# Kernel tuning notes

Hardware: AMD Instinct MI355X
Metric: run time of the kernel (lower is better)

Reference implementation:

```python
import jax, jax.numpy as jnp
import numpy as np
from jax.scipy.optimize import minimize

LAMDA = 0.01        # lamda default in MI()
N_DOMAINS = 2       # domain_label is binary (source/target)
MAXITER = 50        # BFGS iteration budget (torchmin l-bfgs analogue)


def _sq_dists(A, B):
    # squared euclidean pairwise distances == torch.cdist(A, B, p=2) ** 2
    an = jnp.sum(A * A, axis=-1)
    bn = jnp.sum(B * B, axis=-1)
    return an[:, None] + bn[None, :] - 2.0 * (A @ B.T)


def _median_sigma(sf):
    # sigma = median of nonzero squared pairwise source distances.
    # With continuous features the only zeros are the diagonal, so mask it.
    pd = jnp.maximum(_sq_dists(sf, sf), 0.0)
    pd = jnp.where(jnp.eye(pd.shape[0], dtype=bool), jnp.nan, pd)
    return jnp.nanmedian(pd)


def _build(sf, tf, y, l):
    # Gaussian kernel masked by class agreement, plus domain one-hots.
    sigma = _median_sigma(sf)
    X = jnp.concatenate([sf, tf], axis=0)              # [N, d]
    D = _sq_dists(X, X)                                 # [N, N]
    Deltay = (y[:, None] == y[None, :]).astype(X.dtype)
    K_W = jnp.exp(-D / sigma) * Deltay                  # [N, N]
    onehot = jax.nn.one_hot(l[:, 0], N_DOMAINS, dtype=X.dtype)  # [N, 2]
    KD = K_W * (onehot @ onehot.T)                      # K_W * Deltal
    w = jnp.sum(onehot, axis=0) / X.shape[0]            # domain counts / N
    return K_W, KD, onehot, w


def _div(theta, K_W, KD, onehot, w):
    # mean((K_W*Deltal) @ theta) - mean(exp((theta*K_W) @ Deltal - 1))
    # Deltal = onehot @ onehot.T (rank-2), so the second NxN @ NxN matmul
    # collapses to A = K_W @ (theta[:,None]*onehot) with column weights w.
    term1 = jnp.mean(KD @ theta)
    A = K_W @ (theta[:, None] * onehot)                 # [N, 2]
    term2 = jnp.mean(jnp.exp(A - 1.0) @ w)
    return term1 - term2


def _solve_theta(K_W, KD, onehot, w):
    N = K_W.shape[0]
    obj = lambda th: -_div(th, K_W, KD, onehot, w) + LAMDA * (th @ th)
    res = minimize(obj, jnp.zeros((N,), K_W.dtype), method="BFGS",
                   options={"maxiter": MAXITER})
    return res.x


def setup_inputs() -> dict:
    key = jax.random.key(0)
    k1, k2, k3, k4 = jax.random.split(key, 4)
    B, d, n_class = 2048, 256, 31
    source_features = jax.random.normal(k1, (B, d), dtype=jnp.float32)
    target_features = jax.random.normal(k2, (B, d), dtype=jnp.float32)
    y = jax.random.randint(k3, (2 * B,), 0, n_class, dtype=jnp.int32)
    l = jax.random.randint(k4, (2 * B, 1), 0, N_DOMAINS, dtype=jnp.int32)
    return {"source_features": source_features, "target_features": target_features,
            "y": y, "l": l}


def reference(source_features, target_features, y, l):
    K_W, KD, onehot, w = _build(source_features, target_features, y, l)
    theta_hat = _solve_theta(K_W, KD, onehot, w)
    return _div(theta_hat, K_W, KD, onehot, w)
```

## Files before the change

### kernel.cpp

```cpp
#include <hip/hip_runtime.h>
#include <math.h>

#define N_TOT   4096
#define N_SRC   2048
#define DIMF    256
#define NCLASS  31
#define LAMBDA  0.01f

#define K_TRI1  1048063LL
#define K_TRI2  1048064LL

#define WS_ACC    0
#define WS_HIST0  64
#define WS_HISTA  16448
#define WS_HISTB  32832
#define WS_H2A    49216
#define WS_H2B    50240
#define WS_STATE  51264
#define WS_TICK   51520
#define WS_META   52288
#define WS_SCAL   52800
#define ZERO_BYTES 53248
#define WS_PERM   53248
#define WS_XN     69632
#define WS_DS     1048576
#define WS_KBLK   17825792

#define MAXW 224
#define MAXM 112
#define WPAD 116

__device__ __forceinline__ float bf2f(unsigned short h) {
  return __uint_as_float(((unsigned)h) << 16);
}

__device__ __forceinline__ float wredF(float v) {
#pragma unroll
  for (int o = 1; o < 64; o <<= 1) v += __shfl_xor(v, o, 64);
  return v;
}

__device__ __forceinline__ double blockReduceSum(double v, double* red) {
#pragma unroll
  for (int o = 32; o > 0; o >>= 1) v += __shfl_down(v, o, 64);
  int w = threadIdx.x >> 6, lane = threadIdx.x & 63;
  __syncthreads();
  if (lane == 0) red[w] = v;
  __syncthreads();
  return red[0] + red[1] + red[2] + red[3];
}

__device__ __forceinline__ void blockReduceSumMax(double s, double mx, double* red,
                                                  double& os, double& om) {
#pragma unroll
  for (int o = 32; o > 0; o >>= 1) {
    s += __shfl_down(s, o, 64);
    double u = __shfl_down(mx, o, 64);
    mx = fmax(mx, u);
  }
  int w = threadIdx.x >> 6, lane = threadIdx.x & 63;
  __syncthreads();
  if (lane == 0) { red[w] = s; red[4 + w] = mx; }
  __syncthreads();
  os = red[0] + red[1] + red[2] + red[3];
  om = fmax(fmax(red[4], red[5]), fmax(red[6], red[7]));
}

__device__ void scan_find(const unsigned* hist, int nbins, long long k, unsigned* shOut) {
  __shared__ long long tsum[256];
  int tid = threadIdx.x;
  int per = nbins / 256;
  long long s = 0;
  for (int q = 0; q < per; q++) s += hist[tid * per + q];
  tsum[tid] = s;
  __syncthreads();
  long long acc = s;
  for (int off = 1; off < 256; off <<= 1) {
    long long add = (tid >= off) ? tsum[tid - off] : 0;
    __syncthreads();
    acc += add;
    tsum[tid] = acc;
    __syncthreads();
  }
  long long run = acc - s;
  for (int q = 0; q < per; q++) {
    unsigned c = hist[tid * per + q];
    if (k >= run && k < run + (long long)c) { shOut[0] = (unsigned)(tid * per + q); shOut[1] = (unsigned)(k - run); }
    run += c;
  }
  __syncthreads();
}

__global__ __launch_bounds__(256) void xn_kernel(const float* __restrict__ sf,
                                                 const float* __restrict__ tf,
                                                 float* __restrict__ xn) {
  int wid = threadIdx.x >> 6, lane = threadIdx.x & 63;
  int row = blockIdx.x * 4 + wid;
  const float* src = (row < N_SRC) ? (sf + (size_t)row * DIMF) : (tf + (size_t)(row - N_SRC) * DIMF);
  float4 v = ((const float4*)src)[lane];
  float s = v.x * v.x + v.y * v.y + v.z * v.z + v.w * v.w;
#pragma unroll
  for (int o = 32; o > 0; o >>= 1) s += __shfl_down(s, o, 64);
  if (lane == 0) xn[row] = s;
}

__global__ __launch_bounds__(256) void dist_k(const float* __restrict__ sf,
                                              const float* __restrict__ xn,
                                              float* __restrict__ Ds,
                                              unsigned* __restrict__ h) {
  __shared__ float As[16][68];
  __shared__ float Bs[16][68];
  __shared__ unsigned lh[4096];
  const int tx = threadIdx.x, ty = threadIdx.y;
  const int tid = ty * 16 + tx;
  for (int q = tid; q < 4096; q += 256) lh[q] = 0;
  int b = blockIdx.x;
  int by = (int)((sqrtf(8.f * (float)b + 1.f) - 1.f) * 0.5f);
  while ((by + 1) * (by + 2) / 2 <= b) ++by;
  while (by * (by + 1) / 2 > b) --by;
  int bx = b - by * (by + 1) / 2;
  const int R = by * 64, C = bx * 64;
  const int si = tid >> 2, sq = tid & 3;
  float4 va = ((const float4*)(sf + (size_t)(R + si) * 256 + 0))[sq];
  float4 vb = ((const float4*)(sf + (size_t)(C + si) * 256 + 0))[sq];
  float acc[4][4] = {};
  for (int kc = 0; kc < 256; kc += 16) {
    As[sq * 4 + 0][si] = va.x; As[sq * 4 + 1][si] = va.y; As[sq * 4 + 2][si] = va.z; As[sq * 4 + 3][si] = va.w;
    Bs[sq * 4 + 0][si] = vb.x; Bs[sq * 4 + 1][si] = vb.y; Bs[sq * 4 + 2][si] = vb.z; Bs[sq * 4 + 3][si] = vb.w;
    __syncthreads();
    if (kc + 16 < 256) {
      va = ((const float4*)(sf + (size_t)(R + si) * 256 + kc + 16))[sq];
      vb = ((const float4*)(sf + (size_t)(C + si) * 256 + kc + 16))[sq];
    }
#pragma unroll
    for (int k = 0; k < 16; k++) {
      float4 a = *(const float4*)&As[k][ty * 4];
      float4 b2 = *(const float4*)&Bs[k][tx * 4];
      acc[0][0] += a.x * b2.x; acc[0][1] += a.x * b2.y; acc[0][2] += a.x * b2.z; acc[0][3] += a.x * b2.w;
      acc[1][0] += a.y * b2.x; acc[1][1] += a.y * b2.y; acc[1][2] += a.y * b2.z; acc[1][3] += a.y * b2.w;
      acc[2][0] += a.z * b2.x; acc[2][1] += a.z * b2.y; acc[2][2] += a.z * b2.z; acc[2][3] += a.z * b2.w;
      acc[3][0] += a.w * b2.x; acc[3][1] += a.w * b2.y; acc[3][2] += a.w * b2.z; acc[3][3] += a.w * b2.w;
    }
    __syncthreads();
  }
  int jbase = C + tx * 4;
  float xnj0 = xn[jbase + 0], xnj1 = xn[jbase + 1], xnj2 = xn[jbase + 2], xnj3 = xn[jbase + 3];
#pragma unroll
  for (int r = 0; r < 4; r++) {
    int i = R + ty * 4 + r;
    float xni = xn[i];
    float v[4];
    v[0] = fmaxf(xni + xnj0 - 2.f * acc[r][0], 0.f);
    v[1] = fmaxf(xni + xnj1 - 2.f * acc[r][1], 0.f);
    v[2] = fmaxf(xni + xnj2 - 2.f * acc[r][2], 0.f);
    v[3] = fmaxf(xni + xnj3 - 2.f * acc[r][3], 0.f);
    if (jbase + 3 < i) {
      float4 o; o.x = v[0]; o.y = v[1]; o.z = v[2]; o.w = v[3];
      ((float4*)&Ds[(size_t)i * 2048 + jbase])[0] = o;
      atomicAdd(&lh[__float_as_uint(v[0]) >> 20], 1u);
      atomicAdd(&lh[__float_as_uint(v[1]) >> 20], 1u);
      atomicAdd(&lh[__float_as_uint(v[2]) >> 20], 1u);
      atomicAdd(&lh[__float_as_uint(v[3]) >> 20], 1u);
    } else {
#pragma unroll
      for (int k = 0; k < 4; k++) {
        if (jbase + k < i) {
          Ds[(size_t)i * 2048 + jbase + k] = v[k];
          atomicAdd(&lh[__float_as_uint(v[k]) >> 20], 1u);
        }
      }
    }
  }
  __syncthreads();
  for (int q = tid; q < 4096; q += 256) if (lh[q]) atomicAdd(&h[q], lh[q]);
}

__global__ __launch_bounds__(256) void scan0_k(const unsigned* __restrict__ h, unsigned* __restrict__ st) {
  __shared__ unsigned r0[2];
  __shared__ unsigned r1[2];
  scan_find(h, 4096, K_TRI1, r0);
  scan_find(h, 4096, K_TRI2, r1);
  if (threadIdx.x == 0) { st[0] = r0[0]; st[1] = r0[1]; st[2] = r1[0]; st[3] = r1[1]; }
}

__global__ __launch_bounds__(256) void hist1_k(const float* __restrict__ Ds, const unsigned* __restrict__ st,
                                               unsigned* __restrict__ hA, unsigned* __restrict__ hB) {
  __shared__ unsigned lA[4096];
  __shared__ unsigned lB[4096];
  for (int i = threadIdx.x; i < 4096; i += 256) { lA[i] = 0; lB[i] = 0; }
  __syncthreads();
  unsigned s0 = st[0], s1 = st[2];
  int gw = (blockIdx.x * 256 + threadIdx.x) >> 6;
  int lane = threadIdx.x & 63;
  const float* row = Ds + (size_t)gw * 2048;
  for (int j = lane; j < gw; j += 64) {
    unsigned u = __float_as_uint(row[j]);
    unsigned hi = u >> 20, mid = (u >> 8) & 0xFFFu;
    if (hi == s0) atomicAdd(&lA[mid], 1u);
    if (hi == s1) atomicAdd(&lB[mid], 1u);
  }
  __syncthreads();
  for (int i = threadIdx.x; i < 4096; i += 256) {
    if (lA[i]) atomicAdd(&hA[i], lA[i]);
    if (lB[i]) atomicAdd(&hB[i], lB[i]);
  }
}

__global__ __launch_bounds__(256) void scan1_k(const unsigned* __restrict__ hA, const unsigned* __restrict__ hB,
                                               unsigned* __restrict__ st) {
  __shared__ unsigned r0[2];
  __shared__ unsigned r1[2];
  long long kA = (long long)st[1];
  long long kB = (long long)st[3];
  scan_find(hA, 4096, kA, r0);
  scan_find(hB, 4096, kB, r1);
  if (threadIdx.x == 0) { st[4] = r0[0]; st[5] = r0[1]; st[6] = r1[0]; st[7] = r1[1]; }
}

__global__ __launch_bounds__(256) void hist2_k(const float* __restrict__ Ds, const unsigned* __restrict__ st,
                                               unsigned* __restrict__ hA, unsigned* __restrict__ hB) {
  __shared__ unsigned lA[256];
  __shared__ unsigned lB[256];
  lA[threadIdx.x] = 0; lB[threadIdx.x] = 0;
  __syncthreads();
  unsigned p0 = (st[0] << 12) | st[4];
  unsigned p1 = (st[2] << 12) | st[6];
  int gw = (blockIdx.x * 256 + threadIdx.x) >> 6;
  int lane = threadIdx.x & 63;
  const float* row = Ds + (size_t)gw * 2048;
  for (int j = lane; j < gw; j += 64) {
    unsigned u = __float_as_uint(row[j]);
    unsigned pre = u >> 8;
    if (pre == p0) atomicAdd(&lA[u & 0xFFu], 1u);
    if (pre == p1) atomicAdd(&lB[u & 0xFFu], 1u);
  }
  __syncthreads();
  if (lA[threadIdx.x]) atomicAdd(&hA[threadIdx.x], lA[threadIdx.x]);
  if (lB[threadIdx.x]) atomicAdd(&hB[threadIdx.x], lB[threadIdx.x]);
}

__global__ __launch_bounds__(256) void scan2b_k(const unsigned* __restrict__ hA, const unsigned* __restrict__ hB,
                                                const unsigned* __restrict__ st, float* __restrict__ scal,
                                                const int* __restrict__ y, const int* __restrict__ l,
                                                int* __restrict__ perm, int* __restrict__ meta) {
  int tid = threadIdx.x;
  __shared__ unsigned r0[2];
  __shared__ unsigned r1[2];
  scan_find(hA, 256, (long long)st[5], r0);
  scan_find(hB, 256, (long long)st[7], r1);
  if (tid == 0) {
    unsigned v1 = (st[0] << 20) | (st[4] << 8) | r0[0];
    unsigned v2 = (st[2] << 20) | (st[6] << 8) | r1[0];
    scal[0] = 0.5f * (__uint_as_float(v1) + __uint_as_float(v2));
  }
  __shared__ unsigned cl[64];
  __shared__ unsigned bs2[64];
  __shared__ unsigned cur[64];
  if (tid < 64) cl[tid] = 0;
  __syncthreads();
  for (int i = tid; i < N_TOT; i += 256) atomicAdd(&cl[y[i] * 2 + l[i]], 1u);
  __syncthreads();
  if (tid == 0) {
    unsigned run = 0;
    for (int b2 = 0; b2 < 62; b2++) { bs2[b2] = run; run += cl[b2]; }
    unsigned run2 = 0, cnt0 = 0;
    for (int c = 0; c < NCLASS; c++) {
      int n = (int)(cl[2 * c] + cl[2 * c + 1]);
      meta[c] = n; meta[32 + c] = (int)cl[2 * c]; meta[64 + c] = (int)bs2[2 * c];
      meta[96 + c] = (int)run2; run2 += (unsigned)(n * n);
      cnt0 += cl[2 * c];
    }
    scal[1] = (float)((double)cnt0 / (4096.0 * 4096.0));
    scal[2] = (float)((double)(N_TOT - cnt0) / (4096.0 * 4096.0));
  }
  __syncthreads();
  if (tid < 64) cur[tid] = bs2[tid];
  __syncthreads();
  for (int i = tid; i < N_TOT; i += 256) {
    int b2 = y[i] * 2 + l[i];
    unsigned pos = atomicAdd(&cur[b2], 1u);
    perm[pos] = i;
  }
}

__global__ __launch_bounds__(256) void build_k(const float* __restrict__ sf, const float* __restrict__ tf,
                                               const float* __restrict__ xn, const int* __restrict__ perm,
                                               const int* __restrict__ meta, const float* __restrict__ scal,
                                               float* __restrict__ gK) {
  const int c = blockIdx.z;
  const int n = meta[c];
  const int cs = meta[64 + c];
  const int bo = meta[96 + c];
  const int T = (n + 15) >> 4;
  int b = blockIdx.x;
  if (b >= T * (T + 1) / 2) return;
  int by = (int)((sqrtf(8.f * (float)b + 1.f) - 1.f) * 0.5f);
  while ((by + 1) * (by + 2) / 2 <= b) ++by;
  while (by * (by + 1) / 2 > b) --by;
  int bx = b - by * (by + 1) / 2;
  const int i0 = by * 16, j0 = bx * 16;
  const int tx = threadIdx.x, ty = threadIdx.y;
  __shared__ float As[16][260];
  __shared__ float Bs[16][260];
  __shared__ float ot[16][17];
  __shared__ int ra[16];
  __shared__ int rb[16];
  int tid = ty * 16 + tx;
  if (tid < 16) { int il = i0 + tid; ra[tid] = (il < n) ? perm[cs + il] : -1; }
  else if (tid < 32) { int jl = j0 + tid - 16; rb[tid - 16] = (jl < n) ? perm[cs + jl] : -1; }
  __syncthreads();
  for (int e = tid; e < 1024; e += 256) {
    int r = e >> 6, q = e & 63;
    int g = ra[r];
    if (g >= 0) {
      const float* src = (g < N_SRC) ? (sf + (size_t)g * DIMF) : (tf + (size_t)(g - N_SRC) * DIMF);
      ((float4*)&As[r][q * 4])[0] = ((const float4*)src)[q];
    }
    int g2 = rb[r];
    if (g2 >= 0) {
      const float* src = (g2 < N_SRC) ? (sf + (size_t)g2 * DIMF) : (tf + (size_t)(g2 - N_SRC) * DIMF);
      ((float4*)&Bs[r][q * 4])[0] = ((const float4*)src)[q];
    }
  }
  __syncthreads();
  int il = i0 + ty, jl = j0 + tx;
  float val = 0.f;
  if (il < n && jl < n) {
    float dot = 0.f;
    const float4* a4 = (const float4*)&As[ty][0];
    const float4* b4 = (const float4*)&Bs[tx][0];
#pragma unroll 16
    for (int q = 0; q < 64; q++) {
      float4 a = a4[q], b2 = b4[q];
      dot += a.x * b2.x + a.y * b2.y + a.z * b2.z + a.w * b2.w;
    }
    int gi = ra[ty], gj = rb[tx];
    float d = xn[gi] + xn[gj] - 2.f * dot;
    val = expf(-d / scal[0]);
    gK[(size_t)bo + (size_t)il * n + jl] = val;
  }
  ot[ty][tx] = val;
  __syncthreads();
  if (by != bx) {
    int il2 = j0 + ty, jl2 = i0 + tx;
    if (il2 < n && jl2 < n) gK[(size_t)bo + (size_t)il2 * n + jl2] = ot[tx][ty];
  }
}

__global__ __launch_bounds__(256) void solver_k(const float* __restrict__ gK, const int* __restrict__ meta,
                                                const float* __restrict__ scal, double* __restrict__ acc,
                                                unsigned* __restrict__ tick, float* __restrict__ out) {
  const int c = blockIdx.x >> 1, d = blockIdx.x & 1;
  const int n = meta[c];
  const int m0 = meta[32 + c];
  const int m = d ? (n - m0) : m0;
  const int c0 = d ? m0 : 0;
  const int bo = meta[96 + c];
  const float gamma = scal[1 + d];
  const int tid = threadIdx.x;
  const int wv = tid >> 6, lane = tid & 63;

  __shared__ unsigned short Wl[MAXW * WPAD];
  __shared__ float pS[4 * MAXM];
  __shared__ float pD[4 * MAXM];
  __shared__ float Av[MAXW];
  __shared__ float Sv[MAXW];
  __shared__ float Uv[MAXW];
  __shared__ float Bq[MAXW];
  __shared__ float bc[MAXM];
  __shared__ float gv[MAXM];
  __shared__ float dgv[MAXM];
  __shared__ alignas(16) float th[128];
  __shared__ alignas(16) float pv[128];
  __shared__ alignas(16) float xv[128];
  __shared__ double red[16];
  __shared__ double gds[2];
  __shared__ int cgst[2];

  const float* K = gK + bo;
  const int st = n;
  const int mp2 = (m + 1) & ~1;
  const int mp4 = (m + 3) & ~3;
  const int iw0 = (n * wv) >> 2, iw1 = (n * (wv + 1)) >> 2;

  for (int i = tid >> 2; i < n; i += 64) {
    const float* Kr = K + (size_t)i * st + c0;
    unsigned short* Wr = Wl + i * WPAD;
    for (int j = (tid & 3); j < m; j += 4) {
      unsigned u = __float_as_uint(Kr[j]);
      u += 0x7fffu + ((u >> 16) & 1u);
      Wr[j] = (unsigned short)(u >> 16);
    }
    if ((tid & 3) == 0) for (int j = m; j < mp4; j++) Wr[j] = 0;
  }
  {
    const int r0 = (m * wv) >> 2, r1 = (m * (wv + 1)) >> 2;
    for (int j = lane; j < m; j += 64) {
      const float* Kr = K + (size_t)(c0 + j) * st + c0;
      float s = 0.f;
      for (int r = r0; r < r1; r++) s += Kr[r];
      pS[wv * MAXM + j] = s;
    }
  }
  __syncthreads();
  for (int j = tid; j < 128; j += 256) { th[j] = 0.f; pv[j] = 0.f; xv[j] = 0.f; }
  for (int j = tid; j < m; j += 256)
    bc[j] = (pS[j] + pS[MAXM + j] + pS[2 * MAXM + j] + pS[3 * MAXM + j]) * (1.0f / 4096.0f);
  __syncthreads();

  for (int it = 0; it < 25; it++) {
    double o = 0.0;
    if (it == 0) {
      const float s0c = gamma * expf(-1.f);
      for (int i = tid; i < n; i += 256) { Av[i] = 0.f; Sv[i] = s0c; o += (double)s0c; }
    } else {
      for (int i = tid; i < n; i += 256) {
        const unsigned short* Wr = Wl + i * WPAD;
        float a = 0.f;
#pragma unroll 4
        for (int j = 0; j < mp4; j += 4) {
          unsigned long long u = *(const unsigned long long*)(Wr + j);
          float4 t4 = *(const float4*)(th + j);
          unsigned lo = (unsigned)u, hi = (unsigned)(u >> 32);
          a += __uint_as_float(lo << 16) * t4.x
             + __uint_as_float(lo & 0xffff0000u) * t4.y
             + __uint_as_float(hi << 16) * t4.z
             + __uint_as_float(hi & 0xffff0000u) * t4.w;
        }
        Av[i] = a;
        float si = gamma * expf(fminf(a - 1.f, 30.f));
        Sv[i] = si; o += (double)si;
      }
      for (int j = tid; j < m; j += 256) {
        float t_ = th[j];
        o += (double)(-bc[j] * t_ + LAMBDA * t_ * t_);
      }
    }
    __syncthreads();
    if (it == 0) {
      for (int j = lane; j < m; j += 64) {
        const unsigned short* Wc = Wl + j;
        float s_ = 0.f, ds_ = 0.f;
        int i = iw0;
        for (; i + 3 < iw1; i += 4) {
          float w0 = bf2f(Wc[(i + 0) * WPAD]), w1 = bf2f(Wc[(i + 1) * WPAD]);
          float w2 = bf2f(Wc[(i + 2) * WPAD]), w3 = bf2f(Wc[(i + 3) * WPAD]);
          float a0 = w0 * Sv[i], a1 = w1 * Sv[i + 1], a2 = w2 * Sv[i + 2], a3 = w3 * Sv[i + 3];
          s_ += a0 + a1 + a2 + a3;
          ds_ += a0 * w0 + a1 * w1 + a2 * w2 + a3 * w3;
        }
        for (; i < iw1; i++) { float w = bf2f(Wc[i * WPAD]); float a = w * Sv[i]; s_ += a; ds_ += a * w; }
        pS[wv * MAXM + j] = s_; pD[wv * MAXM + j] = ds_;
      }
    } else {
      for (int j = lane; j < m; j += 64) {
        const unsigned short* Wc = Wl + j;
        float s_ = 0.f;
        int i = iw0;
        for (; i + 3 < iw1; i += 4)
          s_ += bf2f(Wc[(i+0)*WPAD]) * Sv[i]   + bf2f(Wc[(i+1)*WPAD]) * Sv[i+1]
              + bf2f(Wc[(i+2)*WPAD]) * Sv[i+2] + bf2f(Wc[(i+3)*WPAD]) * Sv[i+3];
        for (; i < iw1; i++) s_ += bf2f(Wc[i * WPAD]) * Sv[i];
        pS[wv * MAXM + j] = s_;
      }
    }
    __syncthreads();
    double gm = 0.0;
    for (int j = tid; j < m; j += 256) {
      float s_ = pS[j] + pS[MAXM + j] + pS[2 * MAXM + j] + pS[3 * MAXM + j];
      if (it == 0) {
        float ds_ = pD[j] + pD[MAXM + j] + pD[2 * MAXM + j] + pD[3 * MAXM + j];
        dgv[j] = ds_ + 2.f * LAMBDA;
      }
      float g = s_ - bc[j] + 2.f * LAMBDA * th[j];
      gv[j] = g;
      double ag = fabs((double)g); if (ag > gm) gm = ag;
    }
    double obj, gmax;
    blockReduceSumMax(o, gm, red, obj, gmax);
    if (gmax < 1e-5) break;

    const float tolf = (it == 0) ? 1e-2f : ((it == 1) ? 1e-3f : 1e-4f);
    float p0 = 0.f, p1 = 0.f, r0 = 0.f, r1 = 0.f, z0 = 0.f, z1 = 0.f, x0 = 0.f, x1 = 0.f;
    float dg0 = 1.f, dg1 = 1.f, rzf = 0.f, rz0f = 0.f;
    double gtpacc = 0.0;
    const int j0 = lane, j1 = lane + 64;
    if (wv == 0) {
      if (j0 < m) { dg0 = dgv[j0]; r0 = -gv[j0]; z0 = r0 / dg0; }
      if (j1 < m) { dg1 = dgv[j1]; r1 = -gv[j1]; z1 = r1 / dg1; }
      p0 = z0; p1 = z1;
      rzf = wredF(r0 * z0 + r1 * z1);
      rz0f = rzf;
      pv[j0] = p0; pv[j1] = p1;
      if (lane == 0) cgst[0] = (rzf > 0.f) ? 0 : 1;
    }
    __syncthreads();
    for (int cg = 0; cg < 12; cg++) {
      if (cgst[0]) break;
      for (int i = tid; i < n; i += 256) {
        const unsigned short* Wr = Wl + i * WPAD;
        float a = 0.f;
#pragma unroll 4
        for (int j = 0; j < mp4; j += 4) {
          unsigned long long u = *(const unsigned long long*)(Wr + j);
          float4 t4 = *(const float4*)(pv + j);
          unsigned lo = (unsigned)u, hi = (unsigned)(u >> 32);
          a += __uint_as_float(lo << 16) * t4.x
             + __uint_as_float(lo & 0xffff0000u) * t4.y
             + __uint_as_float(hi << 16) * t4.z
             + __uint_as_float(hi & 0xffff0000u) * t4.w;
        }
        Uv[i] = a * Sv[i];
      }
      __syncthreads();
      for (int j = lane; j < m; j += 64) {
        const unsigned short* Wc = Wl + j;
        float q = 0.f;
        int i = iw0;
        for (; i + 3 < iw1; i += 4)
          q += bf2f(Wc[(i+0)*WPAD]) * Uv[i]   + bf2f(Wc[(i+1)*WPAD]) * Uv[i+1]
             + bf2f(Wc[(i+2)*WPAD]) * Uv[i+2] + bf2f(Wc[(i+3)*WPAD]) * Uv[i+3];
        for (; i < iw1; i++) q += bf2f(Wc[i * WPAD]) * Uv[i];
        pS[wv * MAXM + j] = q;
      }
      __syncthreads();
      if (wv == 0) {
        float q0 = 0.f, q1 = 0.f;
        if (j0 < m) q0 = pS[j0] + pS[MAXM + j0] + pS[2*MAXM + j0] + pS[3*MAXM + j0] + 2.f * LAMBDA * p0;
        if (j1 < m) q1 = pS[j1] + pS[MAXM + j1] + pS[2*MAXM + j1] + pS[3*MAXM + j1] + 2.f * LAMBDA * p1;
        float pq = wredF(p0 * q0 + p1 * q1);
        int stop = 0;
        if (!(pq > 0.f)) stop = 1;
        else {
          float alpha = rzf / pq;
          gtpacc += (double)alpha * (double)rzf;
          x0 += alpha * p0; x1 += alpha * p1;
          r0 -= alpha * q0; r1 -= alpha * q1;
          z0 = r0 / dg0;    z1 = r1 / dg1;
          float rzn = wredF(r0 * z0 + r1 * z1);
          if (rzn < tolf * rz0f || cg == 11) stop = 1;
          else {
            float beta = rzn / rzf;
            p0 = z0 + beta * p0; p1 = z1 + beta * p1;
            pv[j0] = p0; pv[j1] = p1;
            rzf = rzn;
          }
        }
        if (lane == 0) cgst[0] = stop;
      }
      __syncthreads();
    }
    if (wv == 0) {
      xv[j0] = x0; xv[j1] = x1;
      if (lane == 0) gds[0] = -gtpacc;
    }
    __syncthreads();
    double gtp = gds[0];
    if (!(gtp < 0.0)) break;

    float t = 1.f;
    if (-gtp >= 1e-4) {
      for (int i = tid; i < n; i += 256) {
        const unsigned short* Wr = Wl + i * WPAD;
        float a = 0.f;
#pragma unroll 4
        for (int j = 0; j < mp4; j += 4) {
          unsigned long long u = *(const unsigned long long*)(Wr + j);
          float4 t4 = *(const float4*)(xv + j);
          unsigned lo = (unsigned)u, hi = (unsigned)(u >> 32);
          a += __uint_as_float(lo << 16) * t4.x
             + __uint_as_float(lo & 0xffff0000u) * t4.y
             + __uint_as_float(hi << 16) * t4.z
             + __uint_as_float(hi & 0xffff0000u) * t4.w;
        }
        Bq[i] = a;
      }
      __syncthreads();
      for (int ls = 0; ls < 10; ls++) {
        double ol = 0.0;
        for (int i = tid; i < n; i += 256)
          ol += (double)(gamma * expf(fminf(Av[i] + t * Bq[i] - 1.f, 30.f)));
        for (int j = tid; j < m; j += 256) {
          float tj = th[j] + t * xv[j];
          ol += (double)(-bc[j] * tj + LAMBDA * tj * tj);
        }
        double ot2 = blockReduceSum(ol, red);
        if (ot2 <= obj + 1e-4 * (double)t * gtp) break;
        t *= 0.5f;
      }
    }
    for (int j = tid; j < mp2; j += 256) th[j] += t * xv[j];
    __syncthreads();
  }

  __syncthreads();
  for (int i = tid; i < n; i += 256) {
    const float* Kr = K + (size_t)i * st + c0;
    float a = 0.f;
    int j = 0;
    for (; j + 7 < m; j += 8)
      a += th[j] * Kr[j] + th[j+1] * Kr[j+1] + th[j+2] * Kr[j+2] + th[j+3] * Kr[j+3]
         + th[j+4] * Kr[j+4] + th[j+5] * Kr[j+5] + th[j+6] * Kr[j+6] + th[j+7] * Kr[j+7];
    for (; j < m; j++) a += th[j] * Kr[j];
    Av[i] = a;
  }
  __syncthreads();
  double t1l = 0.0, t2l = 0.0;
  for (int i = tid; i < n; i += 256) t2l += (double)(gamma * expf(fminf(Av[i] - 1.f, 30.f)));
  for (int j = tid; j < m; j += 256) t1l += (double)(bc[j] * th[j]);
  double t1 = blockReduceSum(t1l, red);
  double t2 = blockReduceSum(t2l, red);
  if (tid == 0) {
    atomicAdd(&acc[0], t1);
    atomicAdd(&acc[1], t2);
    __threadfence();
    unsigned old = __hip_atomic_fetch_add(&tick[0], 1u, __ATOMIC_ACQ_REL, __HIP_MEMORY_SCOPE_AGENT);
    if (old == 61u) {
      double a0 = __hip_atomic_load(&acc[0], __ATOMIC_RELAXED, __HIP_MEMORY_SCOPE_AGENT);
      double a1 = __hip_atomic_load(&acc[1], __ATOMIC_RELAXED, __HIP_MEMORY_SCOPE_AGENT);
      out[0] = (float)(a0 - a1);
    }
  }
}

extern "C" void kernel_launch(void* const* d_in, const int* in_sizes, int n_in,
                              void* d_out, int out_size, void* d_ws, size_t ws_size,
                              hipStream_t stream) {
  const float* sf = (const float*)d_in[0];
  const float* tf = (const float*)d_in[1];
  const int* y = (const int*)d_in[2];
  const int* l = (const int*)d_in[3];
  char* ws = (char*)d_ws;

  double*   acc    = (double*)(ws + WS_ACC);
  unsigned* hist0  = (unsigned*)(ws + WS_HIST0);
  unsigned* histA  = (unsigned*)(ws + WS_HISTA);
  unsigned* histB  = (unsigned*)(ws + WS_HISTB);
  unsigned* h2A    = (unsigned*)(ws + WS_H2A);
  unsigned* h2B    = (unsigned*)(ws + WS_H2B);
  unsigned* state  = (unsigned*)(ws + WS_STATE);
  unsigned* tick   = (unsigned*)(ws + WS_TICK);
  int*      meta   = (int*)(ws + WS_META);
  float*    scal   = (float*)(ws + WS_SCAL);
  int*      perm   = (int*)(ws + WS_PERM);
  float*    xnp    = (float*)(ws + WS_XN);
  float*    Ds     = (float*)(ws + WS_DS);
  float*    gK     = (float*)(ws + WS_KBLK);

  hipMemsetAsync(d_ws, 0, ZERO_BYTES, stream);
  hipLaunchKernelGGL(xn_kernel, dim3(1024), dim3(256), 0, stream, sf, tf, xnp);
  hipLaunchKernelGGL(dist_k, dim3(528), dim3(16, 16), 0, stream, sf, xnp, Ds, hist0);
  hipLaunchKernelGGL(scan0_k, dim3(1), dim3(256), 0, stream, hist0, state);
  hipLaunchKernelGGL(hist1_k, dim3(512), dim3(256), 0, stream, Ds, state, histA, histB);
  hipLaunchKernelGGL(scan1_k, dim3(1), dim3(256), 0, stream, histA, histB, state);
  hipLaunchKernelGGL(hist2_k, dim3(512), dim3(256), 0, stream, Ds, state, h2A, h2B);
  hipLaunchKernelGGL(scan2b_k, dim3(1), dim3(256), 0, stream, h2A, h2B, state, scal, y, l, perm, meta);
  hipLaunchKernelGGL(build_k, dim3(105, 1, NCLASS), dim3(16, 16), 0, stream, sf, tf, xnp, perm, meta, scal, gK);
  hipLaunchKernelGGL(solver_k, dim3(62), dim3(256), 0, stream, gK, meta, scal, acc, tick, (float*)d_out);
}
```

Baseline: 209.3 us.

## Fuse single-block scan kernels into histogram kernels via last-block-done counters

Removes the memset and the three single-block scan kernels by zeroing the workspace inside xn_kernel and having the last block of each histogram kernel (found through an atomic ticket counter) perform the radix-select scan. This cuts four launches and their serialization gaps from the median-selection pipeline. It also merges equal-bin atomics in the distance histogram, and in the solver it spreads row sums and the final K·theta dot products across 4 lanes per row with shuffle reductions. The cost is extra fences and atomics, plus a serial tail where only the last block does the scan.

```diff
diff --git a/kernel.cpp b/kernel.cpp
--- a/kernel.cpp
+++ b/kernel.cpp
@@ -66,9 +66,8 @@
   om = fmax(fmax(red[4], red[5]), fmax(red[6], red[7]));
 }
 
-__device__ void scan_find(const unsigned* hist, int nbins, long long k, unsigned* shOut) {
+__device__ void scan_find(const unsigned* hist, int nbins, long long k, unsigned* shOut, int tid) {
   __shared__ long long tsum[256];
-  int tid = threadIdx.x;
   int per = nbins / 256;
   long long s = 0;
   for (int q = 0; q < per; q++) s += hist[tid * per + q];
@@ -93,7 +92,12 @@
 
 __global__ __launch_bounds__(256) void xn_kernel(const float* __restrict__ sf,
                                                  const float* __restrict__ tf,
-                                                 float* __restrict__ xn) {
+                                                 float* __restrict__ xn,
+                                                 uint4* __restrict__ wsz) {
+  if (blockIdx.x == 0) {
+    uint4 z; z.x = 0; z.y = 0; z.z = 0; z.w = 0;
+    for (int q = threadIdx.x; q < ZERO_BYTES / 16; q += 256) wsz[q] = z;
+  }
   int wid = threadIdx.x >> 6, lane = threadIdx.x & 63;
   int row = blockIdx.x * 4 + wid;
   const float* src = (row < N_SRC) ? (sf + (size_t)row * DIMF) : (tf + (size_t)(row - N_SRC) * DIMF);
@@ -107,10 +111,14 @@
 __global__ __launch_bounds__(256) void dist_k(const float* __restrict__ sf,
                                               const float* __restrict__ xn,
                                               float* __restrict__ Ds,
-                                              unsigned* __restrict__ h) {
+                                              unsigned* __restrict__ h,
+                                              unsigned* __restrict__ st) {
   __shared__ float As[16][68];
   __shared__ float Bs[16][68];
   __shared__ unsigned lh[4096];
+  __shared__ int winner;
+  __shared__ unsigned r0[2];
+  __shared__ unsigned r1[2];
   const int tx = threadIdx.x, ty = threadIdx.y;
   const int tid = ty * 16 + tx;
   for (int q = tid; q < 4096; q += 256) lh[q] = 0;
@@ -157,10 +165,13 @@
     if (jbase + 3 < i) {
       float4 o; o.x = v[0]; o.y = v[1]; o.z = v[2]; o.w = v[3];
       ((float4*)&Ds[(size_t)i * 2048 + jbase])[0] = o;
-      atomicAdd(&lh[__float_as_uint(v[0]) >> 20], 1u);
-      atomicAdd(&lh[__float_as_uint(v[1]) >> 20], 1u);
-      atomicAdd(&lh[__float_as_uint(v[2]) >> 20], 1u);
-      atomicAdd(&lh[__float_as_uint(v[3]) >> 20], 1u);
+      unsigned b0 = __float_as_uint(v[0]) >> 20, b1 = __float_as_uint(v[1]) >> 20;
+      unsigned b2 = __float_as_uint(v[2]) >> 20, b3 = __float_as_uint(v[3]) >> 20;
+      unsigned curb = b0, cnt = 1;
+      if (b1 == curb) cnt++; else { atomicAdd(&lh[curb], cnt); curb = b1; cnt = 1; }
+      if (b2 == curb) cnt++; else { atomicAdd(&lh[curb], cnt); curb = b2; cnt = 1; }
+      if (b3 == curb) cnt++; else { atomicAdd(&lh[curb], cnt); curb = b3; cnt = 1; }
+      atomicAdd(&lh[curb], cnt);
     } else {
 #pragma unroll
       for (int k = 0; k < 4; k++) {
@@ -173,20 +184,28 @@
   }
   __syncthreads();
   for (int q = tid; q < 4096; q += 256) if (lh[q]) atomicAdd(&h[q], lh[q]);
-}
-
-__global__ __launch_bounds__(256) void scan0_k(const unsigned* __restrict__ h, unsigned* __restrict__ st) {
-  __shared__ unsigned r0[2];
-  __shared__ unsigned r1[2];
-  scan_find(h, 4096, K_TRI1, r0);
-  scan_find(h, 4096, K_TRI2, r1);
-  if (threadIdx.x == 0) { st[0] = r0[0]; st[1] = r0[1]; st[2] = r1[0]; st[3] = r1[1]; }
-}
-
-__global__ __launch_bounds__(256) void hist1_k(const float* __restrict__ Ds, const unsigned* __restrict__ st,
+  __threadfence();
+  __syncthreads();
+  if (tid == 0) {
+    unsigned old = __hip_atomic_fetch_add(&st[15], 1u, __ATOMIC_ACQ_REL, __HIP_MEMORY_SCOPE_AGENT);
+    winner = (old == 527u) ? 1 : 0;
+  }
+  __syncthreads();
+  if (winner) {
+    __threadfence();
+    scan_find(h, 4096, K_TRI1, r0, tid);
+    scan_find(h, 4096, K_TRI2, r1, tid);
+    if (tid == 0) { st[0] = r0[0]; st[1] = r0[1]; st[2] = r1[0]; st[3] = r1[1]; }
+  }
+}
+
+__global__ __launch_bounds__(256) void hist1_k(const float* __restrict__ Ds, unsigned* __restrict__ st,
                                                unsigned* __restrict__ hA, unsigned* __restrict__ hB) {
   __shared__ unsigned lA[4096];
   __shared__ unsigned lB[4096];
+  __shared__ int winner;
+  __shared__ unsigned r0[2];
+  __shared__ unsigned r1[2];
   for (int i = threadIdx.x; i < 4096; i += 256) { lA[i] = 0; lB[i] = 0; }
   __syncthreads();
   unsigned s0 = st[0], s1 = st[2];
@@ -204,29 +223,40 @@
     if (lA[i]) atomicAdd(&hA[i], lA[i]);
     if (lB[i]) atomicAdd(&hB[i], lB[i]);
   }
-}
-
-__global__ __launch_bounds__(256) void scan1_k(const unsigned* __restrict__ hA, const unsigned* __restrict__ hB,
-                                               unsigned* __restrict__ st) {
+  __threadfence();
+  __syncthreads();
+  if (threadIdx.x == 0) {
+    unsigned old = __hip_atomic_fetch_add(&st[14], 1u, __ATOMIC_ACQ_REL, __HIP_MEMORY_SCOPE_AGENT);
+    winner = (old == 511u) ? 1 : 0;
+  }
+  __syncthreads();
+  if (winner) {
+    __threadfence();
+    long long kA = (long long)st[1];
+    long long kB = (long long)st[3];
+    scan_find(hA, 4096, kA, r0, threadIdx.x);
+    scan_find(hB, 4096, kB, r1, threadIdx.x);
+    if (threadIdx.x == 0) { st[4] = r0[0]; st[5] = r0[1]; st[6] = r1[0]; st[7] = r1[1]; }
+  }
+}
+
+__global__ __launch_bounds__(256) void hist2_k(const float* __restrict__ Ds, unsigned* __restrict__ st,
+                                               unsigned* __restrict__ hA, unsigned* __restrict__ hB,
+                                               float* __restrict__ scal,
+                                               const int* __restrict__ y, const int* __restrict__ l,
+                                               int* __restrict__ perm, int* __restrict__ meta) {
+  __shared__ unsigned lA[256];
+  __shared__ unsigned lB[256];
+  __shared__ int winner;
   __shared__ unsigned r0[2];
   __shared__ unsigned r1[2];
-  long long kA = (long long)st[1];
-  long long kB = (long long)st[3];
-  scan_find(hA, 4096, kA, r0);
-  scan_find(hB, 4096, kB, r1);
-  if (threadIdx.x == 0) { st[4] = r0[0]; st[5] = r0[1]; st[6] = r1[0]; st[7] = r1[1]; }
-}
-
-__global__ __launch_bounds__(256) void hist2_k(const float* __restrict__ Ds, const unsigned* __restrict__ st,
-                                               unsigned* __restrict__ hA, unsigned* __restrict__ hB) {
-  __shared__ unsigned lA[256];
-  __shared__ unsigned lB[256];
-  lA[threadIdx.x] = 0; lB[threadIdx.x] = 0;
+  int tid = threadIdx.x;
+  lA[tid] = 0; lB[tid] = 0;
   __syncthreads();
   unsigned p0 = (st[0] << 12) | st[4];
   unsigned p1 = (st[2] << 12) | st[6];
-  int gw = (blockIdx.x * 256 + threadIdx.x) >> 6;
-  int lane = threadIdx.x & 63;
+  int gw = (blockIdx.x * 256 + tid) >> 6;
+  int lane = tid & 63;
   const float* row = Ds + (size_t)gw * 2048;
   for (int j = lane; j < gw; j += 64) {
     unsigned u = __float_as_uint(row[j]);
@@ -235,19 +265,19 @@
     if (pre == p1) atomicAdd(&lB[u & 0xFFu], 1u);
   }
   __syncthreads();
-  if (lA[threadIdx.x]) atomicAdd(&hA[threadIdx.x], lA[threadIdx.x]);
-  if (lB[threadIdx.x]) atomicAdd(&hB[threadIdx.x], lB[threadIdx.x]);
-}
-
-__global__ __launch_bounds__(256) void scan2b_k(const unsigned* __restrict__ hA, const unsigned* __restrict__ hB,
-                                                const unsigned* __restrict__ st, float* __restrict__ scal,
-                                                const int* __restrict__ y, const int* __restrict__ l,
-                                                int* __restrict__ perm, int* __restrict__ meta) {
-  int tid = threadIdx.x;
-  __shared__ unsigned r0[2];
-  __shared__ unsigned r1[2];
-  scan_find(hA, 256, (long long)st[5], r0);
-  scan_find(hB, 256, (long long)st[7], r1);
+  if (lA[tid]) atomicAdd(&hA[tid], lA[tid]);
+  if (lB[tid]) atomicAdd(&hB[tid], lB[tid]);
+  __threadfence();
+  __syncthreads();
+  if (tid == 0) {
+    unsigned old = __hip_atomic_fetch_add(&st[12], 1u, __ATOMIC_ACQ_REL, __HIP_MEMORY_SCOPE_AGENT);
+    winner = (old == 511u) ? 1 : 0;
+  }
+  __syncthreads();
+  if (!winner) return;
+  __threadfence();
+  scan_find(hA, 256, (long long)st[5], r0, tid);
+  scan_find(hB, 256, (long long)st[7], r1, tid);
   if (tid == 0) {
     unsigned v1 = (st[0] << 20) | (st[4] << 8) | r0[0];
     unsigned v2 = (st[2] << 20) | (st[6] << 8) | r1[0];
@@ -382,30 +412,28 @@
   const int mp2 = (m + 1) & ~1;
   const int mp4 = (m + 3) & ~3;
   const int iw0 = (n * wv) >> 2, iw1 = (n * (wv + 1)) >> 2;
-
-  for (int i = tid >> 2; i < n; i += 64) {
+  const int rq = tid >> 2, ql = tid & 3;
+
+  for (int i = rq; i < n; i += 64) {
     const float* Kr = K + (size_t)i * st + c0;
     unsigned short* Wr = Wl + i * WPAD;
-    for (int j = (tid & 3); j < m; j += 4) {
+    for (int j = ql; j < m; j += 4) {
       unsigned u = __float_as_uint(Kr[j]);
       u += 0x7fffu + ((u >> 16) & 1u);
       Wr[j] = (unsigned short)(u >> 16);
     }
-    if ((tid & 3) == 0) for (int j = m; j < mp4; j++) Wr[j] = 0;
-  }
-  {
-    const int r0 = (m * wv) >> 2, r1 = (m * (wv + 1)) >> 2;
-    for (int j = lane; j < m; j += 64) {
-      const float* Kr = K + (size_t)(c0 + j) * st + c0;
-      float s = 0.f;
-      for (int r = r0; r < r1; r++) s += Kr[r];
-      pS[wv * MAXM + j] = s;
-    }
+    if (ql == 0) for (int j = m; j < mp4; j++) Wr[j] = 0;
+  }
+  for (int j = rq; j < m; j += 64) {
+    const float* Kr = K + (size_t)(c0 + j) * st + c0;
+    float s = 0.f;
+    for (int r = ql; r < m; r += 4) s += Kr[r];
+    s += __shfl_xor(s, 1, 64);
+    s += __shfl_xor(s, 2, 64);
+    if (ql == 0) bc[j] = s * (1.0f / 4096.0f);
   }
   __syncthreads();
   for (int j = tid; j < 128; j += 256) { th[j] = 0.f; pv[j] = 0.f; xv[j] = 0.f; }
-  for (int j = tid; j < m; j += 256)
-    bc[j] = (pS[j] + pS[MAXM + j] + pS[2 * MAXM + j] + pS[3 * MAXM + j]) * (1.0f / 4096.0f);
   __syncthreads();
 
   for (int it = 0; it < 25; it++) {
@@ -594,15 +622,14 @@
   }
 
   __syncthreads();
-  for (int i = tid; i < n; i += 256) {
+  for (int i = rq; i < n; i += 64) {
     const float* Kr = K + (size_t)i * st + c0;
     float a = 0.f;
-    int j = 0;
-    for (; j + 7 < m; j += 8)
-      a += th[j] * Kr[j] + th[j+1] * Kr[j+1] + th[j+2] * Kr[j+2] + th[j+3] * Kr[j+3]
-         + th[j+4] * Kr[j+4] + th[j+5] * Kr[j+5] + th[j+6] * Kr[j+6] + th[j+7] * Kr[j+7];
-    for (; j < m; j++) a += th[j] * Kr[j];
-    Av[i] = a;
+#pragma unroll 4
+    for (int j = ql; j < m; j += 4) a += th[j] * Kr[j];
+    a += __shfl_xor(a, 1, 64);
+    a += __shfl_xor(a, 2, 64);
+    if (ql == 0) Av[i] = a;
   }
   __syncthreads();
   double t1l = 0.0, t2l = 0.0;
@@ -647,14 +674,10 @@
   float*    Ds     = (float*)(ws + WS_DS);
   float*    gK     = (float*)(ws + WS_KBLK);
 
-  hipMemsetAsync(d_ws, 0, ZERO_BYTES, stream);
-  hipLaunchKernelGGL(xn_kernel, dim3(1024), dim3(256), 0, stream, sf, tf, xnp);
-  hipLaunchKernelGGL(dist_k, dim3(528), dim3(16, 16), 0, stream, sf, xnp, Ds, hist0);
-  hipLaunchKernelGGL(scan0_k, dim3(1), dim3(256), 0, stream, hist0, state);
+  hipLaunchKernelGGL(xn_kernel, dim3(1024), dim3(256), 0, stream, sf, tf, xnp, (uint4*)ws);
+  hipLaunchKernelGGL(dist_k, dim3(528), dim3(16, 16), 0, stream, sf, xnp, Ds, hist0, state);
   hipLaunchKernelGGL(hist1_k, dim3(512), dim3(256), 0, stream, Ds, state, histA, histB);
-  hipLaunchKernelGGL(scan1_k, dim3(1), dim3(256), 0, stream, histA, histB, state);
-  hipLaunchKernelGGL(hist2_k, dim3(512), dim3(256), 0, stream, Ds, state, h2A, h2B);
-  hipLaunchKernelGGL(scan2b_k, dim3(1), dim3(256), 0, stream, h2A, h2B, state, scal, y, l, perm, meta);
+  hipLaunchKernelGGL(hist2_k, dim3(512), dim3(256), 0, stream, Ds, state, h2A, h2B, scal, y, l, perm, meta);
   hipLaunchKernelGGL(build_k, dim3(105, 1, NCLASS), dim3(16, 16), 0, stream, sf, tf, xnp, perm, meta, scal, gK);
   hipLaunchKernelGGL(solver_k, dim3(62), dim3(256), 0, stream, gK, meta, scal, acc, tick, (float*)d_out);
 }
```

Measured after the change: 317.1 us. 1.52x slower.
